# Performance work log

Hardware: AMD Instinct MI355X
Metric: run time of the kernel (lower is better)

Reference implementation:

```python
import jax, jax.numpy as jnp
import numpy as np


COMMITMENT_COST = 0.25


def setup_inputs() -> dict:
    key = jax.random.key(0)
    k1, k2 = jax.random.split(key)
    B, C, H, W = 16, 128, 64, 64
    K = 1024
    z = jax.random.normal(k1, (B, C, H, W), dtype=jnp.float32)
    # original init: uniform(-1/K, 1/K); keep that scale for faithfulness
    codebook = jax.random.uniform(k2, (K, C), dtype=jnp.float32,
                                  minval=-1.0 / K, maxval=1.0 / K)
    return {"z": z, "codebook": codebook}


def reference(z, codebook):
    B, C, H, W = z.shape
    K = codebook.shape[0]
    # (B,C,H,W) -> (N,C) with N = B*H*W
    z_flat = jnp.transpose(z, (0, 2, 3, 1)).reshape(-1, C)
    # squared-distance matrix (N,K): ||z||^2 + ||e||^2 - 2 z.e
    dists = (jnp.sum(z_flat ** 2, axis=1, keepdims=True)
             + jnp.sum(codebook ** 2, axis=1)
             - 2.0 * z_flat @ codebook.T)
    indices = jnp.argmin(dists, axis=1)  # (N,)
    z_q = jnp.transpose(codebook[indices].reshape(B, H, W, C), (0, 3, 1, 2))
    commitment_loss = jnp.mean((jax.lax.stop_gradient(z_q) - z) ** 2)
    codebook_loss = jnp.mean((z_q - jax.lax.stop_gradient(z)) ** 2)
    vq_loss = codebook_loss + COMMITMENT_COST * commitment_loss
    # straight-through estimator
    z_q_st = z + jax.lax.stop_gradient(z_q - z)
    usage = jnp.sum(jnp.bincount(indices, length=K) > 0).astype(jnp.float32) / K
    return (z_q_st, vq_loss, usage)
```

## Files before the change

kernel.cpp:

```cpp
#include <hip/hip_runtime.h>

typedef __attribute__((ext_vector_type(8))) short short8;
typedef __attribute__((ext_vector_type(4))) float f32x4;

#define C_DIM 128
#define K_CODES 1024
#define TOT 8388608
#define NBLK 512

__device__ __forceinline__ unsigned int f2bf1(float f) {
  unsigned int u = __float_as_uint(f);
  return (u + 0x7FFFu + ((u >> 16) & 1u)) >> 16;
}
__device__ __forceinline__ unsigned int f2bf2(float lo, float hi) {
  return f2bf1(lo) | (f2bf1(hi) << 16);
}

union U16x8 { uint4 u; short8 s; };

__global__ void prep_kernel(const float* __restrict__ cb,
                            unsigned short* __restrict__ ebf,
                            float* __restrict__ nsq1,
                            int* __restrict__ used) {
  int gid = blockIdx.x * 256 + threadIdx.x;
  ebf[gid] = (unsigned short)f2bf1(cb[gid]);
  if (gid < K_CODES) {
    float s = 0.f;
    #pragma unroll 8
    for (int c = 0; c < C_DIM; ++c) { float v = cb[gid * C_DIM + c]; s += v * v; }
    nsq1[gid] = 1.0f + s;
    used[gid] = 0;
  }
}

__global__ __launch_bounds__(256, 3)
void vq_main(const float* __restrict__ zin, const float* __restrict__ cb,
             const unsigned short* __restrict__ ebf,
             const float* __restrict__ nsq1,
             int* __restrict__ used, float* __restrict__ lossp,
             float* __restrict__ out) {
  __shared__ __align__(16) uint4 bG[2][1024];
  __shared__ float nsq_s[K_CODES];
  __shared__ unsigned int mergeK[128][2];
  __shared__ int   widx[128];
  __shared__ float wsum[4];

  const int t  = threadIdx.x;
  const int L  = t & 63;
  const int wv = t >> 6;
  const int ph = wv >> 1;
  const int kh = wv & 1;
  const int q  = L >> 4;
  const int nL = L & 15;

  const int bb = blockIdx.x >> 5;
  const int hg = blockIdx.x & 31;
  const int zoff = bb * (C_DIM * 4096) + hg * 128;

  for (int i = t; i < K_CODES; i += 256) nsq_s[i] = nsq1[i];

  short8 afrag[16];
  #pragma unroll
  for (int mt = 0; mt < 4; ++mt) {
    const int wcol = ph * 64 + mt * 16 + nL;
    #pragma unroll
    for (int ks = 0; ks < 4; ++ks) {
      float v[8];
      #pragma unroll
      for (int u = 0; u < 8; ++u)
        v[u] = zin[zoff + (ks * 32 + q * 8 + u) * 4096 + wcol];
      U16x8 pk;
      pk.u.x = f2bf2(-2.f * v[0], -2.f * v[1]);
      pk.u.y = f2bf2(-2.f * v[2], -2.f * v[3]);
      pk.u.z = f2bf2(-2.f * v[4], -2.f * v[5]);
      pk.u.w = f2bf2(-2.f * v[6], -2.f * v[7]);
      afrag[mt * 4 + ks] = pk.s;
    }
  }

  const uint4* __restrict__ ebv = (const uint4*)ebf;
  const int nLw = t >> 4;
  const int oct = t & 15;
  const int sks = oct >> 2, sq = oct & 3;

  #pragma unroll
  for (int p = 0; p < 4; ++p) {
    int r = p * 16 + nLw;
    bG[0][p * 256 + sks * 64 + nLw * 4 + sq] = ebv[r * 16 + oct];
  }
  __syncthreads();

  unsigned int kmin[16];
  #pragma unroll
  for (int i = 0; i < 16; ++i) kmin[i] = 0xFFFFFFFFu;

  #pragma unroll 1
  for (int ch = 0; ch < 16; ++ch) {
    const int cur = ch & 1;
    if (ch < 15) {
      #pragma unroll
      for (int p = 0; p < 4; ++p) {
        int r = p * 16 + nLw;
        bG[cur ^ 1][p * 256 + sks * 64 + nLw * 4 + sq] =
            ebv[((ch + 1) * 64 + r) * 16 + oct];
      }
    }
    const short8* bp = (const short8*)bG[cur];
    #pragma unroll
    for (int j2 = 0; j2 < 2; ++j2) {
      const int jj = kh * 2 + j2;
      const int row = ch * 64 + jj * 16 + nL;
      short8 b0 = bp[jj * 256 + 0 * 64 + nL * 4 + q];
      short8 b1 = bp[jj * 256 + 1 * 64 + nL * 4 + q];
      short8 b2 = bp[jj * 256 + 2 * 64 + nL * 4 + q];
      short8 b3 = bp[jj * 256 + 3 * 64 + nL * 4 + q];
      const float nv = nsq_s[row];
      f32x4 a0 = {nv, nv, nv, nv};
      f32x4 a1 = {nv, nv, nv, nv};
      f32x4 a2 = {nv, nv, nv, nv};
      f32x4 a3 = {nv, nv, nv, nv};
      a0 = __builtin_amdgcn_mfma_f32_16x16x32_bf16(afrag[0],  b0, a0, 0, 0, 0);
      a1 = __builtin_amdgcn_mfma_f32_16x16x32_bf16(afrag[4],  b0, a1, 0, 0, 0);
      a2 = __builtin_amdgcn_mfma_f32_16x16x32_bf16(afrag[8],  b0, a2, 0, 0, 0);
      a3 = __builtin_amdgcn_mfma_f32_16x16x32_bf16(afrag[12], b0, a3, 0, 0, 0);
      a0 = __builtin_amdgcn_mfma_f32_16x16x32_bf16(afrag[1],  b1, a0, 0, 0, 0);
      a1 = __builtin_amdgcn_mfma_f32_16x16x32_bf16(afrag[5],  b1, a1, 0, 0, 0);
      a2 = __builtin_amdgcn_mfma_f32_16x16x32_bf16(afrag[9],  b1, a2, 0, 0, 0);
      a3 = __builtin_amdgcn_mfma_f32_16x16x32_bf16(afrag[13], b1, a3, 0, 0, 0);
      a0 = __builtin_amdgcn_mfma_f32_16x16x32_bf16(afrag[2],  b2, a0, 0, 0, 0);
      a1 = __builtin_amdgcn_mfma_f32_16x16x32_bf16(afrag[6],  b2, a1, 0, 0, 0);
      a2 = __builtin_amdgcn_mfma_f32_16x16x32_bf16(afrag[10], b2, a2, 0, 0, 0);
      a3 = __builtin_amdgcn_mfma_f32_16x16x32_bf16(afrag[14], b2, a3, 0, 0, 0);
      a0 = __builtin_amdgcn_mfma_f32_16x16x32_bf16(afrag[3],  b3, a0, 0, 0, 0);
      a1 = __builtin_amdgcn_mfma_f32_16x16x32_bf16(afrag[7],  b3, a1, 0, 0, 0);
      a2 = __builtin_amdgcn_mfma_f32_16x16x32_bf16(afrag[11], b3, a2, 0, 0, 0);
      a3 = __builtin_amdgcn_mfma_f32_16x16x32_bf16(afrag[15], b3, a3, 0, 0, 0);
      const unsigned int rowc = (unsigned int)row;
      #pragma unroll
      for (int r = 0; r < 4; ++r) {
        unsigned int k0 = (__float_as_uint(a0[r]) & 0xFFFFFC00u) | rowc;
        if (k0 < kmin[r]) kmin[r] = k0;
        unsigned int k1 = (__float_as_uint(a1[r]) & 0xFFFFFC00u) | rowc;
        if (k1 < kmin[4 + r]) kmin[4 + r] = k1;
        unsigned int k2 = (__float_as_uint(a2[r]) & 0xFFFFFC00u) | rowc;
        if (k2 < kmin[8 + r]) kmin[8 + r] = k2;
        unsigned int k3 = (__float_as_uint(a3[r]) & 0xFFFFFC00u) | rowc;
        if (k3 < kmin[12 + r]) kmin[12 + r] = k3;
      }
    }
    __syncthreads();
  }

  #pragma unroll
  for (int m = 1; m <= 8; m <<= 1) {
    #pragma unroll
    for (int i = 0; i < 16; ++i) {
      unsigned int o = (unsigned int)__shfl_xor((int)kmin[i], m, 64);
      if (o < kmin[i]) kmin[i] = o;
    }
  }
  if (nL == 0) {
    #pragma unroll
    for (int mt = 0; mt < 4; ++mt)
      #pragma unroll
      for (int r = 0; r < 4; ++r)
        mergeK[ph * 64 + mt * 16 + q * 4 + r][kh] = kmin[mt * 4 + r];
  }
  __syncthreads();

  if (t < 128) {
    unsigned int b = min(mergeK[t][0], mergeK[t][1]);
    int bi = (int)(b & 1023u);
    widx[t] = bi;
    used[bi] = 1;
  }
  __syncthreads();

  float lsum = 0.f;
  {
    const int p = t & 127, cg = t >> 7;
    const int idx = widx[p];
    const uint4* erow = ebv + idx * 16 + cg * 8;
    const int obase = zoff + cg * 64 * 4096 + p;
    #pragma unroll 2
    for (int i = 0; i < 8; ++i) {
      uint4 g = erow[i];
      const unsigned int wrd[4] = {g.x, g.y, g.z, g.w};
      #pragma unroll
      for (int half = 0; half < 4; ++half) {
        float e0 = __uint_as_float(wrd[half] << 16);
        float e1 = __uint_as_float(wrd[half] & 0xFFFF0000u);
        int off = obase + (i * 8 + half * 2) * 4096;
        float d0 = zin[off] - e0;
        out[off] = e0;
        lsum += d0 * d0;
        off += 4096;
        float d1 = zin[off] - e1;
        out[off] = e1;
        lsum += d1 * d1;
      }
    }
  }
  #pragma unroll
  for (int o = 32; o > 0; o >>= 1) lsum += __shfl_down(lsum, o, 64);
  if (L == 0) wsum[wv] = lsum;
  __syncthreads();
  if (t == 0) lossp[blockIdx.x] = wsum[0] + wsum[1] + wsum[2] + wsum[3];
}

__global__ void finalize_kernel(const int* __restrict__ used,
                                const float* __restrict__ lossp,
                                float* __restrict__ out2) {
  __shared__ int   redi[256];
  __shared__ float redf[256];
  int t = threadIdx.x;
  int s = 0;
  for (int i = t; i < K_CODES; i += 256) s += (used[i] != 0) ? 1 : 0;
  float ls = 0.f;
  for (int i = t; i < NBLK; i += 256) ls += lossp[i];
  redi[t] = s; redf[t] = ls;
  __syncthreads();
  for (int o = 128; o > 0; o >>= 1) {
    if (t < o) { redi[t] += redi[t + o]; redf[t] += redf[t + o]; }
    __syncthreads();
  }
  if (t == 0) {
    out2[0] = 1.25f * redf[0] / (float)TOT;
    out2[1] = (float)redi[0] / 1024.0f;
  }
}

extern "C" void kernel_launch(void* const* d_in, const int* in_sizes, int n_in,
                              void* d_out, int out_size, void* d_ws, size_t ws_size,
                              hipStream_t stream) {
  const float* z  = (const float*)d_in[0];
  const float* cb = (const float*)d_in[1];
  float* out = (float*)d_out;
  char* ws = (char*)d_ws;
  unsigned short* ebf = (unsigned short*)ws;
  float* nsq1  = (float*)(ws + 262144);
  int*   used  = (int*)(ws + 266240);
  float* lossp = (float*)(ws + 270336);

  hipLaunchKernelGGL(prep_kernel, dim3(512), dim3(256), 0, stream,
                     cb, ebf, nsq1, used);
  hipLaunchKernelGGL(vq_main, dim3(NBLK), dim3(256), 0, stream,
                     z, cb, ebf, nsq1, used, lossp, out);
  hipLaunchKernelGGL(finalize_kernel, dim3(1), dim3(256), 0, stream,
                     used, lossp, out + TOT);
}
```

Before: 117.5 us.

## Stage z in LDS, pre-swizzle codebook, reuse staged z in epilogue

The prep kernel now also writes a bf16 codebook copy already arranged in the MFMA-friendly LDS layout, so each chunk load in the main kernel becomes a contiguous copy. The main kernel converts each z tile to bf16 once into a swizzled LDS buffer, shared by all waves rather than loaded redundantly per wave. The epilogue computes the loss from this staged bf16 z instead of re-reading fp32 z from global memory, removing a full second pass over the input. Codebook prefetch is split so global loads are issued before the MFMA work and the LDS stores happen after it. In exchange, LDS use grows by 32 KB per block, which may lower occupancy, and the loss is now computed from bf16-rounded z values, which reduces its accuracy.

```diff
diff --git a/kernel.cpp b/kernel.cpp
--- a/kernel.cpp
+++ b/kernel.cpp
@@ -16,30 +16,36 @@
   return f2bf1(lo) | (f2bf1(hi) << 16);
 }
 
-union U16x8 { uint4 u; short8 s; };
-
 __global__ void prep_kernel(const float* __restrict__ cb,
                             unsigned short* __restrict__ ebf,
+                            unsigned short* __restrict__ ebsw,
                             float* __restrict__ nsq1,
                             int* __restrict__ used) {
   int gid = blockIdx.x * 256 + threadIdx.x;
-  ebf[gid] = (unsigned short)f2bf1(cb[gid]);
+  unsigned short b = (unsigned short)f2bf1(cb[gid]);
+  ebf[gid] = b;
+  int r = gid >> 7, c = gid & 127;
+  int ks = c >> 5, q = (c >> 3) & 3, u = c & 7;
+  int dstg = (r >> 6) * 1024 + ((r >> 4) & 3) * 256 + ks * 64 + (r & 15) * 4 + q;
+  ebsw[dstg * 8 + u] = b;
   if (gid < K_CODES) {
     float s = 0.f;
     #pragma unroll 8
-    for (int c = 0; c < C_DIM; ++c) { float v = cb[gid * C_DIM + c]; s += v * v; }
+    for (int cc = 0; cc < C_DIM; ++cc) { float v = cb[gid * C_DIM + cc]; s += v * v; }
     nsq1[gid] = 1.0f + s;
     used[gid] = 0;
   }
 }
 
 __global__ __launch_bounds__(256, 3)
-void vq_main(const float* __restrict__ zin, const float* __restrict__ cb,
+void vq_main(const float* __restrict__ zin,
              const unsigned short* __restrict__ ebf,
+             const unsigned short* __restrict__ ebsw,
              const float* __restrict__ nsq1,
              int* __restrict__ used, float* __restrict__ lossp,
              float* __restrict__ out) {
   __shared__ __align__(16) uint4 bG[2][1024];
+  __shared__ __align__(16) uint4 zG[2048];
   __shared__ float nsq_s[K_CODES];
   __shared__ unsigned int mergeK[128][2];
   __shared__ int   widx[128];
@@ -59,36 +65,43 @@
 
   for (int i = t; i < K_CODES; i += 256) nsq_s[i] = nsq1[i];
 
+  const uint4* __restrict__ esw = (const uint4*)ebsw;
+  const uint4* __restrict__ ebv = (const uint4*)ebf;
+
+  #pragma unroll
+  for (int p = 0; p < 4; ++p) bG[0][p * 256 + t] = esw[p * 256 + t];
+  {
+    const int w = t & 127;
+    const int pt = w >> 4, mL = w & 15;
+    #pragma unroll
+    for (int p = 0; p < 8; ++p) {
+      const int oct = p * 2 + (t >> 7);
+      const int ks = oct >> 2, qq = oct & 3;
+      float v[8];
+      #pragma unroll
+      for (int u = 0; u < 8; ++u)
+        v[u] = zin[zoff + (oct * 8 + u) * 4096 + w];
+      uint4 val;
+      val.x = f2bf2(-2.f * v[0], -2.f * v[1]);
+      val.y = f2bf2(-2.f * v[2], -2.f * v[3]);
+      val.z = f2bf2(-2.f * v[4], -2.f * v[5]);
+      val.w = f2bf2(-2.f * v[6], -2.f * v[7]);
+      zG[ks * 512 + pt * 64 + qq * 16 + ((mL + 4 * (pt + qq)) & 15)] = val;
+    }
+  }
+  __syncthreads();
+
   short8 afrag[16];
-  #pragma unroll
-  for (int mt = 0; mt < 4; ++mt) {
-    const int wcol = ph * 64 + mt * 16 + nL;
-    #pragma unroll
-    for (int ks = 0; ks < 4; ++ks) {
-      float v[8];
-      #pragma unroll
-      for (int u = 0; u < 8; ++u)
-        v[u] = zin[zoff + (ks * 32 + q * 8 + u) * 4096 + wcol];
-      U16x8 pk;
-      pk.u.x = f2bf2(-2.f * v[0], -2.f * v[1]);
-      pk.u.y = f2bf2(-2.f * v[2], -2.f * v[3]);
-      pk.u.z = f2bf2(-2.f * v[4], -2.f * v[5]);
-      pk.u.w = f2bf2(-2.f * v[6], -2.f * v[7]);
-      afrag[mt * 4 + ks] = pk.s;
-    }
-  }
-
-  const uint4* __restrict__ ebv = (const uint4*)ebf;
-  const int nLw = t >> 4;
-  const int oct = t & 15;
-  const int sks = oct >> 2, sq = oct & 3;
-
-  #pragma unroll
-  for (int p = 0; p < 4; ++p) {
-    int r = p * 16 + nLw;
-    bG[0][p * 256 + sks * 64 + nLw * 4 + sq] = ebv[r * 16 + oct];
-  }
-  __syncthreads();
+  {
+    const short8* zp = (const short8*)zG;
+    #pragma unroll
+    for (int mt = 0; mt < 4; ++mt) {
+      const int pt = ph * 4 + mt;
+      #pragma unroll
+      for (int ks = 0; ks < 4; ++ks)
+        afrag[mt * 4 + ks] = zp[ks * 512 + pt * 64 + q * 16 + ((nL + 4 * (pt + q)) & 15)];
+    }
+  }
 
   unsigned int kmin[16];
   #pragma unroll
@@ -97,13 +110,10 @@
   #pragma unroll 1
   for (int ch = 0; ch < 16; ++ch) {
     const int cur = ch & 1;
+    uint4 st[4];
     if (ch < 15) {
       #pragma unroll
-      for (int p = 0; p < 4; ++p) {
-        int r = p * 16 + nLw;
-        bG[cur ^ 1][p * 256 + sks * 64 + nLw * 4 + sq] =
-            ebv[((ch + 1) * 64 + r) * 16 + oct];
-      }
+      for (int p = 0; p < 4; ++p) st[p] = esw[(ch + 1) * 1024 + p * 256 + t];
     }
     const short8* bp = (const short8*)bG[cur];
     #pragma unroll
@@ -148,6 +158,10 @@
         if (k3 < kmin[12 + r]) kmin[12 + r] = k3;
       }
     }
+    if (ch < 15) {
+      #pragma unroll
+      for (int p = 0; p < 4; ++p) bG[cur ^ 1][p * 256 + t] = st[p];
+    }
     __syncthreads();
   }
 
@@ -180,24 +194,26 @@
   {
     const int p = t & 127, cg = t >> 7;
     const int idx = widx[p];
-    const uint4* erow = ebv + idx * 16 + cg * 8;
-    const int obase = zoff + cg * 64 * 4096 + p;
+    const int pt = p >> 4, mL = p & 15;
+    const int obase = zoff + p;
     #pragma unroll 2
-    for (int i = 0; i < 8; ++i) {
-      uint4 g = erow[i];
-      const unsigned int wrd[4] = {g.x, g.y, g.z, g.w};
-      #pragma unroll
-      for (int half = 0; half < 4; ++half) {
-        float e0 = __uint_as_float(wrd[half] << 16);
-        float e1 = __uint_as_float(wrd[half] & 0xFFFF0000u);
-        int off = obase + (i * 8 + half * 2) * 4096;
-        float d0 = zin[off] - e0;
+    for (int j8 = 0; j8 < 8; ++j8) {
+      const int ks = cg * 2 + (j8 >> 2), qq = j8 & 3;
+      uint4 eg = ebv[idx * 16 + ks * 4 + qq];
+      uint4 zg = zG[ks * 512 + pt * 64 + qq * 16 + ((mL + 4 * (pt + qq)) & 15)];
+      const unsigned int ew[4] = {eg.x, eg.y, eg.z, eg.w};
+      const unsigned int zw[4] = {zg.x, zg.y, zg.z, zg.w};
+      #pragma unroll
+      for (int hw = 0; hw < 4; ++hw) {
+        float e0 = __uint_as_float(ew[hw] << 16);
+        float e1 = __uint_as_float(ew[hw] & 0xFFFF0000u);
+        float z0 = -0.5f * __uint_as_float(zw[hw] << 16);
+        float z1 = -0.5f * __uint_as_float(zw[hw] & 0xFFFF0000u);
+        int off = obase + (ks * 32 + qq * 8 + hw * 2) * 4096;
         out[off] = e0;
-        lsum += d0 * d0;
-        off += 4096;
-        float d1 = zin[off] - e1;
-        out[off] = e1;
-        lsum += d1 * d1;
+        float d0 = z0 - e0; lsum += d0 * d0;
+        out[off + 4096] = e1;
+        float d1 = z1 - e1; lsum += d1 * d1;
       }
     }
   }
@@ -237,15 +253,16 @@
   const float* cb = (const float*)d_in[1];
   float* out = (float*)d_out;
   char* ws = (char*)d_ws;
-  unsigned short* ebf = (unsigned short*)ws;
-  float* nsq1  = (float*)(ws + 262144);
-  int*   used  = (int*)(ws + 266240);
-  float* lossp = (float*)(ws + 270336);
+  unsigned short* ebf  = (unsigned short*)ws;
+  unsigned short* ebsw = (unsigned short*)(ws + 262144);
+  float* nsq1  = (float*)(ws + 524288);
+  int*   used  = (int*)(ws + 528384);
+  float* lossp = (float*)(ws + 532480);
 
   hipLaunchKernelGGL(prep_kernel, dim3(512), dim3(256), 0, stream,
-                     cb, ebf, nsq1, used);
+                     cb, ebf, ebsw, nsq1, used);
   hipLaunchKernelGGL(vq_main, dim3(NBLK), dim3(256), 0, stream,
-                     z, cb, ebf, nsq1, used, lossp, out);
+                     z, ebf, ebsw, nsq1, used, lossp, out);
   hipLaunchKernelGGL(finalize_kernel, dim3(1), dim3(256), 0, stream,
                      used, lossp, out + TOT);
 }
```

New measurement: 133.4 us. 1.14x slower.
